# Optimization experiments

Measured on AMD Instinct MI355X. Metric: run time of the kernel, lower is better.

The kernel has to match this reference:

```python
import jax, jax.numpy as jnp
import numpy as np

D = 120000   # sample_size
H1 = 600     # sample_size/200
H2 = 300     # sample_size/400
H3 = 200     # sample_size/600
DENSITY = 0.1  # sparselinear default connectivity
B = 512
EPS = 1e-5

_LAYER_SPECS = [(H1, D), (H1, H1), (H2, H1), (H3, H2), (H3, H3)]


def _make_idx(key, out_d, in_d, nnz):
    k1, k2 = jax.random.split(key)
    rows = jax.random.randint(k1, (nnz,), 0, out_d)
    cols = jax.random.randint(k2, (nnz,), 0, in_d)
    return jnp.stack([rows, cols]).astype(jnp.int32)


def setup_inputs() -> dict:
    key = jax.random.key(0)
    ks = jax.random.split(key, 32)
    inp = {"x": jax.random.normal(ks[0], (B, D), jnp.float32)}
    for i, (o, ii) in enumerate(_LAYER_SPECS, 1):
        nnz = int(DENSITY * o * ii)
        scale = 1.0 / np.sqrt(DENSITY * ii)  # kaiming-like fan-in scaling on nonzeros
        inp[f"idx{i}"] = _make_idx(ks[3 * i], o, ii, nnz)
        inp[f"val{i}"] = jax.random.normal(ks[3 * i + 1], (nnz,), jnp.float32) * scale
        inp[f"b{i}"] = jnp.zeros((o,), jnp.float32)
    for j, d in enumerate([H1, H2, H3], 1):
        inp[f"g{j}"] = jnp.ones((d,), jnp.float32)
        inp[f"be{j}"] = jnp.zeros((d,), jnp.float32)
    return inp


def _sp_linear(x, idx, vals, bias, out_d):
    # COO sparse linear: y = x @ W^T + b, W scattered from (row, col, val)
    in_d = x.shape[1]
    W = jnp.zeros((out_d, in_d), x.dtype).at[idx[0], idx[1]].add(vals)
    return x @ W.T + bias


def _bn(x, g, b):
    # BatchNorm1d, training mode: biased batch variance
    m = x.mean(axis=0)
    v = x.var(axis=0)
    return (x - m) * jax.lax.rsqrt(v + EPS) * g + b


def reference(x, idx1, val1, b1, idx2, val2, b2, idx3, val3, b3,
              idx4, val4, b4, idx5, val5, b5,
              g1, be1, g2, be2, g3, be3):
    h = jax.nn.silu(_bn(_sp_linear(x, idx1, val1, b1, H1), g1, be1))
    h = jax.nn.silu(_sp_linear(h, idx2, val2, b2, H1))
    h = jax.nn.silu(_bn(_sp_linear(h, idx3, val3, b3, H2), g2, be2))
    h = jax.nn.silu(_bn(_sp_linear(h, idx4, val4, b4, H3), g3, be3))
    return _sp_linear(h, idx5, val5, b5, H3)
```

## Files before the change

### kernel.cpp

```cpp
#include <hip/hip_runtime.h>

typedef unsigned short ushort_t;
typedef unsigned int uint_t;

typedef __bf16 bf16x8 __attribute__((ext_vector_type(8)));
typedef float  floatx4 __attribute__((ext_vector_type(4)));

#define AS3 __attribute__((address_space(3)))
#define AS1 __attribute__((address_space(1)))

#define BATCH 512
#define D_IN  120000
#define N1P   640
#define N2P   640
#define N3P   320
#define N4P   256
#define N5P   256

static constexpr long O_W1 = 0;
static constexpr long SZ_W1 = 640L * 120000 * 2;
static constexpr long O_W2 = O_W1 + SZ_W1;
static constexpr long SZ_W2 = 640L * 640 * 4;
static constexpr long O_W3 = O_W2 + SZ_W2;
static constexpr long SZ_W3 = 320L * 640 * 4;
static constexpr long O_W4 = O_W3 + SZ_W3;
static constexpr long SZ_W4 = 256L * 320 * 4;
static constexpr long O_W5 = O_W4 + SZ_W4;
static constexpr long SZ_W5 = 256L * 256 * 4;
static constexpr long O_Y1 = O_W5 + SZ_W5;
static constexpr long SZ_Y1 = 512L * 640 * 4;
static constexpr long ZERO_BYTES = O_Y1 + SZ_Y1;
static constexpr long O_XB = ZERO_BYTES;
static constexpr long SZ_XB = 512L * 120000 * 2;
static constexpr long O_H1 = O_XB;
static constexpr long O_H2 = O_H1 + 512L * 640 * 4;
static constexpr long O_Y3 = O_H2 + 512L * 640 * 4;
static constexpr long O_H3 = O_Y3 + 512L * 320 * 4;
static constexpr long O_Y4 = O_H3 + 512L * 320 * 4;
static constexpr long O_H4 = O_Y4 + 512L * 256 * 4;

__device__ __forceinline__ ushort_t f2bf(float f) {
    union { float f; uint_t u; } x;
    x.f = f;
    uint_t u = x.u;
    return (ushort_t)((u + 0x7FFFu + ((u >> 16) & 1u)) >> 16);
}
__device__ __forceinline__ float bf2f(ushort_t h) {
    union { uint_t u; float f; } x;
    x.u = ((uint_t)h) << 16;
    return x.f;
}
__device__ __forceinline__ float silu_f(float z) {
    return z / (1.f + expf(-z));
}
__device__ __forceinline__ void load16_lds(const void* g, void* l) {
    __builtin_amdgcn_global_load_lds((const AS1 char*)g, (AS3 char*)l, 16, 0, 0);
}

__global__ void zero_f4(float4* __restrict__ p, long n4) {
    long stride = (long)gridDim.x * blockDim.x;
    for (long i = (long)blockIdx.x * blockDim.x + threadIdx.x; i < n4; i += stride)
        p[i] = make_float4(0.f, 0.f, 0.f, 0.f);
}

__global__ void cast_f32_bf16(const float* __restrict__ X, ushort_t* __restrict__ Xb, long n8) {
    long t = (long)blockIdx.x * blockDim.x + threadIdx.x;
    if (t >= n8) return;
    const float4* p = (const float4*)X + 2 * t;
    float4 a = p[0], b = p[1];
    union { ushort_t us[8]; uint4 v; } u;
    u.us[0] = f2bf(a.x); u.us[1] = f2bf(a.y); u.us[2] = f2bf(a.z); u.us[3] = f2bf(a.w);
    u.us[4] = f2bf(b.x); u.us[5] = f2bf(b.y); u.us[6] = f2bf(b.z); u.us[7] = f2bf(b.w);
    ((uint4*)Xb)[t] = u.v;
}

__global__ void scatter_bf16(const int* __restrict__ idx, const float* __restrict__ vals,
                             int nnz, ushort_t* __restrict__ W, int ldw) {
    int i = blockIdx.x * blockDim.x + threadIdx.x;
    if (i >= nnz) return;
    int r = idx[i];
    int c = idx[nnz + i];
    float v = vals[i];
    size_t e = (size_t)r * ldw + c;
    uint_t* word = (uint_t*)((char*)W + ((e * 2) & ~(size_t)3));
    bool hi = (e & 1);
    uint_t cur = *word, assumed;
    do {
        assumed = cur;
        ushort_t h = hi ? (ushort_t)(assumed >> 16) : (ushort_t)(assumed & 0xFFFFu);
        ushort_t nh = f2bf(bf2f(h) + v);
        uint_t nw = hi ? ((assumed & 0x0000FFFFu) | ((uint_t)nh << 16))
                       : ((assumed & 0xFFFF0000u) | (uint_t)nh);
        cur = atomicCAS(word, assumed, nw);
    } while (cur != assumed);
}

__global__ void scatter_f32(const int* __restrict__ idx, const float* __restrict__ vals,
                            int nnz, float* __restrict__ W, int ldw) {
    int i = blockIdx.x * blockDim.x + threadIdx.x;
    if (i >= nnz) return;
    atomicAdd(&W[(size_t)idx[i] * ldw + idx[nnz + i]], vals[i]);
}

__global__ __launch_bounds__(256) void gemm1(const ushort_t* __restrict__ X,
                                             const ushort_t* __restrict__ W,
                                             float* __restrict__ Y, int kChunk) {
    __shared__ ushort_t sA[128 * 32];
    __shared__ ushort_t sB[128 * 32];

    const int tile = blockIdx.x;
    const int bm = tile / 5, bn = tile % 5;
    const int ks = blockIdx.y * kChunk;
    const int iters = kChunk / 32;

    const int t = threadIdx.x;
    const int lane = t & 63;
    const int w = t >> 6;
    const int wm = w >> 1, wn = w & 1;

    const int c0 = w * 128 + lane;
    const int c1 = c0 + 64;
    const int rA0 = c0 >> 2, qA0 = c0 & 3;
    const int rA1 = c1 >> 2, qA1 = c1 & 3;

    const ushort_t* pa0 = X + (size_t)(bm * 128 + rA0) * D_IN + ks + qA0 * 8;
    const ushort_t* pa1 = X + (size_t)(bm * 128 + rA1) * D_IN + ks + qA1 * 8;
    const ushort_t* pb0 = W + (size_t)(bn * 128 + rA0) * D_IN + ks + qA0 * 8;
    const ushort_t* pb1 = W + (size_t)(bn * 128 + rA1) * D_IN + ks + qA1 * 8;

    ushort_t* la0 = sA + (size_t)(w * 128) * 8;
    ushort_t* la1 = sA + (size_t)(w * 128 + 64) * 8;
    ushort_t* lb0 = sB + (size_t)(w * 128) * 8;
    ushort_t* lb1 = sB + (size_t)(w * 128 + 64) * 8;

    const int i16 = lane & 15;
    const int qk = lane >> 4;
    const bf16x8* ap[4];
    const bf16x8* bp[4];
#pragma unroll
    for (int mi = 0; mi < 4; mi++)
        ap[mi] = (const bf16x8*)&sA[(size_t)(wm * 64 + mi * 16 + i16) * 32 + qk * 8];
#pragma unroll
    for (int ni = 0; ni < 4; ni++)
        bp[ni] = (const bf16x8*)&sB[(size_t)(wn * 64 + ni * 16 + i16) * 32 + qk * 8];

    floatx4 acc[4][4] = {};

    for (int it = 0; it < iters; ++it) {
        __syncthreads();
        load16_lds(pa0, la0);
        load16_lds(pa1, la1);
        load16_lds(pb0, lb0);
        load16_lds(pb1, lb1);
        pa0 += 32; pa1 += 32; pb0 += 32; pb1 += 32;
        __syncthreads();

        bf16x8 af[4], bfr[4];
#pragma unroll
        for (int mi = 0; mi < 4; mi++) af[mi] = *ap[mi];
#pragma unroll
        for (int ni = 0; ni < 4; ni++) bfr[ni] = *bp[ni];
#pragma unroll
        for (int mi = 0; mi < 4; mi++)
#pragma unroll
            for (int ni = 0; ni < 4; ni++)
                acc[mi][ni] = __builtin_amdgcn_mfma_f32_16x16x32_bf16(af[mi], bfr[ni], acc[mi][ni], 0, 0, 0);
    }

#pragma unroll
    for (int mi = 0; mi < 4; mi++) {
#pragma unroll
        for (int ni = 0; ni < 4; ni++) {
#pragma unroll
            for (int r = 0; r < 4; r++) {
                int row = bm * 128 + wm * 64 + mi * 16 + qk * 4 + r;
                int col = bn * 128 + wn * 64 + ni * 16 + i16;
                atomicAdd(&Y[(size_t)row * N1P + col], acc[mi][ni][r]);
            }
        }
    }
}

__global__ void bn_silu(const float* __restrict__ Y, int ld, int realN,
                        const float* __restrict__ g, const float* __restrict__ be,
                        float* __restrict__ H) {
    int j = blockIdx.x;
    int t = threadIdx.x;
    if (j >= realN) {
        for (int b = t; b < BATCH; b += 256) H[(size_t)b * ld + j] = 0.f;
        return;
    }
    float v0 = Y[(size_t)t * ld + j];
    float v1 = Y[(size_t)(t + 256) * ld + j];
    __shared__ float rs[256], rss[256];
    rs[t] = v0 + v1;
    rss[t] = v0 * v0 + v1 * v1;
    __syncthreads();
    for (int o = 128; o > 0; o >>= 1) {
        if (t < o) { rs[t] += rs[t + o]; rss[t] += rss[t + o]; }
        __syncthreads();
    }
    float mean = rs[0] * (1.f / 512.f);
    float var  = rss[0] * (1.f / 512.f) - mean * mean;
    float sc = rsqrtf(var + 1e-5f) * g[j];
    float sh = be[j] - mean * sc;
    H[(size_t)t * ld + j]         = silu_f(v0 * sc + sh);
    H[(size_t)(t + 256) * ld + j] = silu_f(v1 * sc + sh);
}

template <int ACT, int GUARD>
__global__ __launch_bounds__(256) void small_gemm(const float* __restrict__ A, int lda,
                                                  const float* __restrict__ W, int ldw,
                                                  const float* __restrict__ bias, int biasN,
                                                  float* __restrict__ out, int ldo, int outN,
                                                  int K) {
    __shared__ float sA[64][20];
    __shared__ float sB[64][20];
    const int t = threadIdx.x;
    const int m0 = blockIdx.x * 64, n0 = blockIdx.y * 64;
    const int ty = t >> 4, tx = t & 15;
    const int lm = t >> 2, lq = t & 3;
    float acc[4][4] = {};

    for (int kt = 0; kt < K; kt += 16) {
        __syncthreads();
        float4 av = *(const float4*)&A[(size_t)(m0 + lm) * lda + kt + lq * 4];
        float4 wv = *(const float4*)&W[(size_t)(n0 + lm) * ldw + kt + lq * 4];
        sA[lm][lq * 4 + 0] = av.x; sA[lm][lq * 4 + 1] = av.y;
        sA[lm][lq * 4 + 2] = av.z; sA[lm][lq * 4 + 3] = av.w;
        sB[lm][lq * 4 + 0] = wv.x; sB[lm][lq * 4 + 1] = wv.y;
        sB[lm][lq * 4 + 2] = wv.z; sB[lm][lq * 4 + 3] = wv.w;
        __syncthreads();
#pragma unroll
        for (int kg = 0; kg < 4; kg++) {
            float4 a4[4], b4[4];
#pragma unroll
            for (int i = 0; i < 4; i++) a4[i] = *(const float4*)&sA[ty * 4 + i][kg * 4];
#pragma unroll
            for (int j = 0; j < 4; j++) b4[j] = *(const float4*)&sB[tx * 4 + j][kg * 4];
#pragma unroll
            for (int i = 0; i < 4; i++)
#pragma unroll
                for (int j = 0; j < 4; j++)
                    acc[i][j] += a4[i].x * b4[j].x + a4[i].y * b4[j].y +
                                 a4[i].z * b4[j].z + a4[i].w * b4[j].w;
        }
    }

#pragma unroll
    for (int i = 0; i < 4; i++) {
#pragma unroll
        for (int j = 0; j < 4; j++) {
            int row = m0 + ty * 4 + i;
            int col = n0 + tx * 4 + j;
            float v = acc[i][j];
            if (bias != nullptr && col < biasN) v += bias[col];
            if (ACT == 1) v = silu_f(v);
            if (GUARD) {
                if (col < outN) out[(size_t)row * ldo + col] = v;
            } else {
                out[(size_t)row * ldo + col] = v;
            }
        }
    }
}

extern "C" void kernel_launch(void* const* d_in, const int* in_sizes, int n_in,
                              void* d_out, int out_size, void* d_ws, size_t ws_size,
                              hipStream_t stream) {
    const float* x   = (const float*)d_in[0];
    const int* idx1 = (const int*)d_in[1];  const float* val1 = (const float*)d_in[2];
    const int* idx2 = (const int*)d_in[4];  const float* val2 = (const float*)d_in[5];
    const float* b2 = (const float*)d_in[6];
    const int* idx3 = (const int*)d_in[7];  const float* val3 = (const float*)d_in[8];
    const int* idx4 = (const int*)d_in[10]; const float* val4 = (const float*)d_in[11];
    const int* idx5 = (const int*)d_in[13]; const float* val5 = (const float*)d_in[14];
    const float* b5 = (const float*)d_in[15];
    const float* g1 = (const float*)d_in[16]; const float* be1 = (const float*)d_in[17];
    const float* g2 = (const float*)d_in[18]; const float* be2 = (const float*)d_in[19];
    const float* g3 = (const float*)d_in[20]; const float* be3 = (const float*)d_in[21];

    const int nnz1 = in_sizes[1] / 2;
    const int nnz2 = in_sizes[4] / 2;
    const int nnz3 = in_sizes[7] / 2;
    const int nnz4 = in_sizes[10] / 2;
    const int nnz5 = in_sizes[13] / 2;

    char* ws = (char*)d_ws;
    ushort_t* W1 = (ushort_t*)(ws + O_W1);
    float* W2 = (float*)(ws + O_W2);
    float* W3 = (float*)(ws + O_W3);
    float* W4 = (float*)(ws + O_W4);
    float* W5 = (float*)(ws + O_W5);
    float* y1 = (float*)(ws + O_Y1);
    ushort_t* Xb = (ushort_t*)(ws + O_XB);
    float* h1 = (float*)(ws + O_H1);
    float* h2 = (float*)(ws + O_H2);
    float* y3 = (float*)(ws + O_Y3);
    float* h3 = (float*)(ws + O_H3);
    float* y4 = (float*)(ws + O_Y4);
    float* h4 = (float*)(ws + O_H4);

    zero_f4<<<dim3(2048), dim3(256), 0, stream>>>((float4*)ws, ZERO_BYTES / 16);

    {
        long n8 = (long)BATCH * D_IN / 8;
        cast_f32_bf16<<<dim3((unsigned)((n8 + 255) / 256)), dim3(256), 0, stream>>>(x, Xb, n8);
    }

    scatter_bf16<<<dim3((nnz1 + 255) / 256), dim3(256), 0, stream>>>(idx1, val1, nnz1, W1, D_IN);
    scatter_f32<<<dim3((nnz2 + 255) / 256), dim3(256), 0, stream>>>(idx2, val2, nnz2, W2, 640);
    scatter_f32<<<dim3((nnz3 + 255) / 256), dim3(256), 0, stream>>>(idx3, val3, nnz3, W3, 640);
    scatter_f32<<<dim3((nnz4 + 255) / 256), dim3(256), 0, stream>>>(idx4, val4, nnz4, W4, 320);
    scatter_f32<<<dim3((nnz5 + 255) / 256), dim3(256), 0, stream>>>(idx5, val5, nnz5, W5, 256);

    gemm1<<<dim3(20, 30), dim3(256), 0, stream>>>(Xb, W1, y1, 4000);

    bn_silu<<<dim3(N1P), dim3(256), 0, stream>>>(y1, N1P, 600, g1, be1, h1);

    small_gemm<1, 0><<<dim3(8, N2P / 64), dim3(256), 0, stream>>>(h1, N1P, W2, 640, b2, 600,
                                                                  h2, N2P, N2P, 640);
    small_gemm<0, 0><<<dim3(8, N3P / 64), dim3(256), 0, stream>>>(h2, N2P, W3, 640, nullptr, 0,
                                                                  y3, N3P, N3P, 640);
    bn_silu<<<dim3(N3P), dim3(256), 0, stream>>>(y3, N3P, 300, g2, be2, h3);

    small_gemm<0, 0><<<dim3(8, N4P / 64), dim3(256), 0, stream>>>(h3, N3P, W4, 320, nullptr, 0,
                                                                  y4, N4P, N4P, 320);
    bn_silu<<<dim3(N4P), dim3(256), 0, stream>>>(y4, N4P, 200, g3, be3, h4);

    small_gemm<0, 1><<<dim3(8, N5P / 64), dim3(256), 0, stream>>>(h4, N4P, W5, 256, b5, 200,
                                                                  (float*)d_out, 200, 200, 256);
    (void)n_in; (void)out_size; (void)ws_size;
}
```

Before: 1.173 ms.

## Build W1 via bucketed LDS accumulation and use split-K partials instead of atomics

Replaces zeroing the dense bf16 W1 plus a global CAS-loop scatter with two steps. The COO entries are first bucketed by row and column slice, then each slice is accumulated in shared memory and written densely, so W1 needs no zeroing. The input cast is split into two halves so the bf16 copy of x is half the size. gemm1 writes per-split partial sums with plain stores, and a separate reduction kernel sums them in place of float atomics. This adds a bucket buffer, a fixed bucket capacity that silently drops overflow entries, and rounding of values to bf16 before they are summed. W1 now holds only 600 rows, so the padded GEMM tile reads rows 600-639 from the adjacent workspace, and those results land only in discarded padding columns.

Result: slower. 1.706 ms (+45.5%).

```diff
diff --git a/kernel.cpp b/kernel.cpp
--- a/kernel.cpp
+++ b/kernel.cpp
@@ -17,21 +17,35 @@
 #define N4P   256
 #define N5P   256
 
-static constexpr long O_W1 = 0;
-static constexpr long SZ_W1 = 640L * 120000 * 2;
-static constexpr long O_W2 = O_W1 + SZ_W1;
+#define SUBS  8
+#define SUBW  15000
+#define NBKT  (600 * SUBS)
+#define BCAP  2048
+
+#define NSPLIT 25
+#define KCHUNK 2400
+
+static constexpr long O_W1  = 0;
+static constexpr long SZ_W1 = 600L * D_IN * 2;
+static constexpr long O_BKT = O_W1 + SZ_W1;
+static constexpr long SZ_BKT = (long)NBKT * BCAP * 4;
+static constexpr long O_PART = O_BKT;
+static constexpr long O_Y1  = O_BKT + SZ_BKT;
+static constexpr long SZ_Y1 = 512L * N1P * 4;
+static constexpr long O_W2  = O_Y1 + SZ_Y1;
 static constexpr long SZ_W2 = 640L * 640 * 4;
-static constexpr long O_W3 = O_W2 + SZ_W2;
+static constexpr long O_W3  = O_W2 + SZ_W2;
 static constexpr long SZ_W3 = 320L * 640 * 4;
-static constexpr long O_W4 = O_W3 + SZ_W3;
+static constexpr long O_W4  = O_W3 + SZ_W3;
 static constexpr long SZ_W4 = 256L * 320 * 4;
-static constexpr long O_W5 = O_W4 + SZ_W4;
+static constexpr long O_W5  = O_W4 + SZ_W4;
 static constexpr long SZ_W5 = 256L * 256 * 4;
-static constexpr long O_Y1 = O_W5 + SZ_W5;
-static constexpr long SZ_Y1 = 512L * 640 * 4;
-static constexpr long ZERO_BYTES = O_Y1 + SZ_Y1;
-static constexpr long O_XB = ZERO_BYTES;
-static constexpr long SZ_XB = 512L * 120000 * 2;
+static constexpr long O_CUR = O_W5 + SZ_W5;
+static constexpr long SZ_CUR = (long)NBKT * 4;
+static constexpr long ZERO_OFF = O_W2;
+static constexpr long ZERO_BYTES = SZ_W2 + SZ_W3 + SZ_W4 + SZ_W5 + SZ_CUR;
+static constexpr long O_XB  = O_CUR + SZ_CUR;
+static constexpr long SZ_XB = 512L * 60000 * 2;
 static constexpr long O_H1 = O_XB;
 static constexpr long O_H2 = O_H1 + 512L * 640 * 4;
 static constexpr long O_Y3 = O_H2 + 512L * 640 * 4;
@@ -58,41 +72,48 @@
 }
 
 __global__ void zero_f4(float4* __restrict__ p, long n4) {
-    long stride = (long)gridDim.x * blockDim.x;
-    for (long i = (long)blockIdx.x * blockDim.x + threadIdx.x; i < n4; i += stride)
-        p[i] = make_float4(0.f, 0.f, 0.f, 0.f);
-}
-
-__global__ void cast_f32_bf16(const float* __restrict__ X, ushort_t* __restrict__ Xb, long n8) {
-    long t = (long)blockIdx.x * blockDim.x + threadIdx.x;
-    if (t >= n8) return;
-    const float4* p = (const float4*)X + 2 * t;
-    float4 a = p[0], b = p[1];
-    union { ushort_t us[8]; uint4 v; } u;
-    u.us[0] = f2bf(a.x); u.us[1] = f2bf(a.y); u.us[2] = f2bf(a.z); u.us[3] = f2bf(a.w);
-    u.us[4] = f2bf(b.x); u.us[5] = f2bf(b.y); u.us[6] = f2bf(b.z); u.us[7] = f2bf(b.w);
-    ((uint4*)Xb)[t] = u.v;
-}
-
-__global__ void scatter_bf16(const int* __restrict__ idx, const float* __restrict__ vals,
-                             int nnz, ushort_t* __restrict__ W, int ldw) {
+    long i = (long)blockIdx.x * blockDim.x + threadIdx.x;
+    if (i < n4) p[i] = make_float4(0.f, 0.f, 0.f, 0.f);
+}
+
+__global__ void reorder(const int* __restrict__ idx, const float* __restrict__ vals,
+                        int nnz, uint_t* __restrict__ bkt, int* __restrict__ cur) {
     int i = blockIdx.x * blockDim.x + threadIdx.x;
     if (i >= nnz) return;
     int r = idx[i];
     int c = idx[nnz + i];
-    float v = vals[i];
-    size_t e = (size_t)r * ldw + c;
-    uint_t* word = (uint_t*)((char*)W + ((e * 2) & ~(size_t)3));
-    bool hi = (e & 1);
-    uint_t cur = *word, assumed;
-    do {
-        assumed = cur;
-        ushort_t h = hi ? (ushort_t)(assumed >> 16) : (ushort_t)(assumed & 0xFFFFu);
-        ushort_t nh = f2bf(bf2f(h) + v);
-        uint_t nw = hi ? ((assumed & 0x0000FFFFu) | ((uint_t)nh << 16))
-                       : ((assumed & 0xFFFF0000u) | (uint_t)nh);
-        cur = atomicCAS(word, assumed, nw);
-    } while (cur != assumed);
+    int q = c / SUBW;
+    int b = r * SUBS + q;
+    int colw = c - q * SUBW;
+    int pos = atomicAdd(&cur[b], 1);
+    if (pos < BCAP)
+        bkt[(size_t)b * BCAP + pos] = ((uint_t)colw << 16) | (uint_t)f2bf(vals[i]);
+}
+
+__global__ __launch_bounds__(256) void fill_w1(const uint_t* __restrict__ bkt,
+                                               const int* __restrict__ cur,
+                                               ushort_t* __restrict__ W) {
+    __shared__ float acc[SUBW];
+    const int b = blockIdx.x;
+    const int t = threadIdx.x;
+    for (int i = t; i < SUBW; i += 256) acc[i] = 0.f;
+    __syncthreads();
+    int cnt = cur[b];
+    if (cnt > BCAP) cnt = BCAP;
+    const uint_t* p = bkt + (size_t)b * BCAP;
+    for (int i = t; i < cnt; i += 256) {
+        uint_t e = p[i];
+        atomicAdd(&acc[e >> 16], bf2f((ushort_t)(e & 0xFFFFu)));
+    }
+    __syncthreads();
+    const int r = b >> 3, sub = b & 7;
+    ushort_t* dst = W + (size_t)r * D_IN + sub * SUBW;
+    for (int i = t; i < SUBW / 8; i += 256) {
+        union { ushort_t us[8]; uint4 v; } u;
+#pragma unroll
+        for (int k = 0; k < 8; k++) u.us[k] = f2bf(acc[i * 8 + k]);
+        ((uint4*)dst)[i] = u.v;
+    }
 }
 
 __global__ void scatter_f32(const int* __restrict__ idx, const float* __restrict__ vals,
@@ -102,16 +123,28 @@
     atomicAdd(&W[(size_t)idx[i] * ldw + idx[nnz + i]], vals[i]);
 }
 
-__global__ __launch_bounds__(256) void gemm1(const ushort_t* __restrict__ X,
-                                             const ushort_t* __restrict__ W,
-                                             float* __restrict__ Y, int kChunk) {
+__global__ void cast_half(const float* __restrict__ X, int kbase, ushort_t* __restrict__ Xb) {
+    long t = (long)blockIdx.x * blockDim.x + threadIdx.x;
+    if (t >= (long)BATCH * 7500) return;
+    int row = (int)(t / 7500);
+    int c8 = (int)(t - (long)row * 7500);
+    const float4* s = (const float4*)(X + (size_t)row * D_IN + kbase + c8 * 8);
+    float4 a = s[0], bb = s[1];
+    union { ushort_t us[8]; uint4 v; } u;
+    u.us[0] = f2bf(a.x);  u.us[1] = f2bf(a.y);  u.us[2] = f2bf(a.z);  u.us[3] = f2bf(a.w);
+    u.us[4] = f2bf(bb.x); u.us[5] = f2bf(bb.y); u.us[6] = f2bf(bb.z); u.us[7] = f2bf(bb.w);
+    ((uint4*)Xb)[t] = u.v;
+}
+
+__global__ __launch_bounds__(256) void gemm1(const ushort_t* __restrict__ X, int ldx,
+                                             const ushort_t* __restrict__ W, int kwbase,
+                                             float* __restrict__ P, int accum) {
     __shared__ ushort_t sA[128 * 32];
     __shared__ ushort_t sB[128 * 32];
 
     const int tile = blockIdx.x;
     const int bm = tile / 5, bn = tile % 5;
-    const int ks = blockIdx.y * kChunk;
-    const int iters = kChunk / 32;
+    const int ks = blockIdx.y * KCHUNK;
 
     const int t = threadIdx.x;
     const int lane = t & 63;
@@ -123,10 +156,10 @@
     const int rA0 = c0 >> 2, qA0 = c0 & 3;
     const int rA1 = c1 >> 2, qA1 = c1 & 3;
 
-    const ushort_t* pa0 = X + (size_t)(bm * 128 + rA0) * D_IN + ks + qA0 * 8;
-    const ushort_t* pa1 = X + (size_t)(bm * 128 + rA1) * D_IN + ks + qA1 * 8;
-    const ushort_t* pb0 = W + (size_t)(bn * 128 + rA0) * D_IN + ks + qA0 * 8;
-    const ushort_t* pb1 = W + (size_t)(bn * 128 + rA1) * D_IN + ks + qA1 * 8;
+    const ushort_t* pa0 = X + (size_t)(bm * 128 + rA0) * ldx + ks + qA0 * 8;
+    const ushort_t* pa1 = X + (size_t)(bm * 128 + rA1) * ldx + ks + qA1 * 8;
+    const ushort_t* pb0 = W + (size_t)(bn * 128 + rA0) * D_IN + kwbase + ks + qA0 * 8;
+    const ushort_t* pb1 = W + (size_t)(bn * 128 + rA1) * D_IN + kwbase + ks + qA1 * 8;
 
     ushort_t* la0 = sA + (size_t)(w * 128) * 8;
     ushort_t* la1 = sA + (size_t)(w * 128 + 64) * 8;
@@ -146,7 +179,7 @@
 
     floatx4 acc[4][4] = {};
 
-    for (int it = 0; it < iters; ++it) {
+    for (int it = 0; it < KCHUNK / 32; ++it) {
         __syncthreads();
         load16_lds(pa0, la0);
         load16_lds(pa1, la1);
@@ -167,6 +200,7 @@
                 acc[mi][ni] = __builtin_amdgcn_mfma_f32_16x16x32_bf16(af[mi], bfr[ni], acc[mi][ni], 0, 0, 0);
     }
 
+    float* Pp = P + (size_t)blockIdx.y * (512 * N1P);
 #pragma unroll
     for (int mi = 0; mi < 4; mi++) {
 #pragma unroll
@@ -175,10 +209,20 @@
             for (int r = 0; r < 4; r++) {
                 int row = bm * 128 + wm * 64 + mi * 16 + qk * 4 + r;
                 int col = bn * 128 + wn * 64 + ni * 16 + i16;
-                atomicAdd(&Y[(size_t)row * N1P + col], acc[mi][ni][r]);
+                size_t o = (size_t)row * N1P + col;
+                if (accum) Pp[o] += acc[mi][ni][r];
+                else       Pp[o]  = acc[mi][ni][r];
             }
         }
     }
+}
+
+__global__ void reduce_part(const float* __restrict__ P, float* __restrict__ Y) {
+    int i = blockIdx.x * 256 + threadIdx.x;
+    float s = 0.f;
+#pragma unroll
+    for (int k = 0; k < NSPLIT; k++) s += P[(size_t)k * (512 * N1P) + i];
+    Y[i] = s;
 }
 
 __global__ void bn_silu(const float* __restrict__ Y, int ld, int realN,
@@ -288,11 +332,14 @@
 
     char* ws = (char*)d_ws;
     ushort_t* W1 = (ushort_t*)(ws + O_W1);
+    uint_t* bkt  = (uint_t*)(ws + O_BKT);
+    float* part  = (float*)(ws + O_PART);
+    float* y1 = (float*)(ws + O_Y1);
     float* W2 = (float*)(ws + O_W2);
     float* W3 = (float*)(ws + O_W3);
     float* W4 = (float*)(ws + O_W4);
     float* W5 = (float*)(ws + O_W5);
-    float* y1 = (float*)(ws + O_Y1);
+    int*   cur = (int*)(ws + O_CUR);
     ushort_t* Xb = (ushort_t*)(ws + O_XB);
     float* h1 = (float*)(ws + O_H1);
     float* h2 = (float*)(ws + O_H2);
@@ -301,20 +348,24 @@
     float* y4 = (float*)(ws + O_Y4);
     float* h4 = (float*)(ws + O_H4);
 
-    zero_f4<<<dim3(2048), dim3(256), 0, stream>>>((float4*)ws, ZERO_BYTES / 16);
-
-    {
-        long n8 = (long)BATCH * D_IN / 8;
-        cast_f32_bf16<<<dim3((unsigned)((n8 + 255) / 256)), dim3(256), 0, stream>>>(x, Xb, n8);
-    }
-
-    scatter_bf16<<<dim3((nnz1 + 255) / 256), dim3(256), 0, stream>>>(idx1, val1, nnz1, W1, D_IN);
+    zero_f4<<<dim3((unsigned)((ZERO_BYTES / 16 + 255) / 256)), dim3(256), 0, stream>>>(
+        (float4*)(ws + ZERO_OFF), ZERO_BYTES / 16);
+
+    reorder<<<dim3((nnz1 + 255) / 256), dim3(256), 0, stream>>>(idx1, val1, nnz1, bkt, cur);
+
+    fill_w1<<<dim3(NBKT), dim3(256), 0, stream>>>(bkt, cur, W1);
+
     scatter_f32<<<dim3((nnz2 + 255) / 256), dim3(256), 0, stream>>>(idx2, val2, nnz2, W2, 640);
     scatter_f32<<<dim3((nnz3 + 255) / 256), dim3(256), 0, stream>>>(idx3, val3, nnz3, W3, 640);
     scatter_f32<<<dim3((nnz4 + 255) / 256), dim3(256), 0, stream>>>(idx4, val4, nnz4, W4, 320);
     scatter_f32<<<dim3((nnz5 + 255) / 256), dim3(256), 0, stream>>>(idx5, val5, nnz5, W5, 256);
 
-    gemm1<<<dim3(20, 30), dim3(256), 0, stream>>>(Xb, W1, y1, 4000);
+    cast_half<<<dim3(15000), dim3(256), 0, stream>>>(x, 0, Xb);
+    gemm1<<<dim3(20, NSPLIT), dim3(256), 0, stream>>>(Xb, 60000, W1, 0, part, 0);
+    cast_half<<<dim3(15000), dim3(256), 0, stream>>>(x, 60000, Xb);
+    gemm1<<<dim3(20, NSPLIT), dim3(256), 0, stream>>>(Xb, 60000, W1, 60000, part, 1);
+
+    reduce_part<<<dim3(512 * N1P / 256), dim3(256), 0, stream>>>(part, y1);
 
     bn_silu<<<dim3(N1P), dim3(256), 0, stream>>>(y1, N1P, 600, g1, be1, h1);
 
```
